# Optimization experiments

Measured on AMD Instinct MI355X. Metric: run time of the kernel, lower is better.

Reference implementation:

```python
import jax, jax.numpy as jnp
import numpy as np

B, E, S = 2, 1024, 2048
H = 16
D_QK = D_V = D_OUT = 1024
NEG = -1e4


def setup_inputs() -> dict:
    key = jax.random.key(0)
    ks = jax.random.split(key, 12)
    q = jax.random.normal(ks[0], (B, E, 1, S), jnp.float32)
    k = jax.random.normal(ks[1], (B, E, 1, S), jnp.float32)
    v = jax.random.normal(ks[2], (B, E, 1, S), jnp.float32)
    # causal qk_mask: (B, src, 1, tgt); src index > tgt index is masked
    causal = jnp.where(jnp.arange(S)[:, None] > jnp.arange(S)[None, :], NEG, 0.0).astype(jnp.float32)
    qk_mask = jnp.broadcast_to(causal[None, :, None, :], (B, S, 1, S))
    k_mask = jnp.zeros((B, S, 1, 1), jnp.float32)
    sc = 1.0 / np.sqrt(E)
    Wq = jax.random.normal(ks[3], (D_QK, E), jnp.float32) * sc
    Wk = jax.random.normal(ks[4], (D_QK, E), jnp.float32) * sc
    Wv = jax.random.normal(ks[5], (D_V, E), jnp.float32) * sc
    Wo = jax.random.normal(ks[6], (D_OUT, D_V), jnp.float32) * sc
    bq = jnp.zeros((D_QK,), jnp.float32)
    bk = jnp.zeros((D_QK,), jnp.float32)
    bv = jnp.zeros((D_V,), jnp.float32)
    bo = jnp.zeros((D_OUT,), jnp.float32)
    return {"q": q, "k": k, "v": v, "qk_mask": qk_mask, "k_mask": k_mask,
            "Wq": Wq, "bq": bq, "Wk": Wk, "bk": bk, "Wv": Wv, "bv": bv,
            "Wo": Wo, "bo": bo}


def reference(q, k, v, qk_mask, k_mask, Wq, bq, Wk, bk, Wv, bv, Wo, bo):
    b, _, _, tq = q.shape
    sk = k.shape[3]
    d_qk, d_v = Wq.shape[0], Wv.shape[0]
    dh, dvh = d_qk // H, d_v // H
    fact = float(dh) ** (-0.5)
    # 1x1 conv projections on (B, C, 1, S) == matmul over channels
    qp = jnp.einsum('oc,bcis->bois', Wq, q) + bq[None, :, None, None]
    kp = jnp.einsum('oc,bcis->bois', Wk, k) + bk[None, :, None, None]
    vp = jnp.einsum('oc,bcis->bois', Wv, v) + bv[None, :, None, None]
    # split heads: channel dim is head-major (contiguous chunks)
    qh = qp[:, :, 0, :].reshape(b, H, dh, tq)
    kh = kp[:, :, 0, :].reshape(b, H, dh, sk)
    vh = vp[:, :, 0, :].reshape(b, H, dvh, sk)
    # scores: (B, H, src, tgt); masks broadcast over heads
    scores = jnp.einsum('bhcq,bhck->bhkq', qh, kh) * fact
    scores = scores + qk_mask[:, None, :, 0, :] + k_mask[:, None, :, 0, 0][..., None]
    w = jax.nn.softmax(scores, axis=2)  # softmax over src (k) axis
    attn = jnp.einsum('bhkq,bhck->bhcq', w, vh).reshape(b, d_v, 1, tq)
    out = jnp.einsum('oc,bcis->bois', Wo, attn) + bo[None, :, None, None]
    return out
```

## Files before the change

kernel.cpp:

```cpp
#include <hip/hip_runtime.h>
#include <hip/hip_bf16.h>
#include <stdint.h>

typedef unsigned short u16;
typedef __attribute__((ext_vector_type(8))) short short8;
typedef __attribute__((ext_vector_type(4))) short short4v;
typedef __attribute__((ext_vector_type(4))) float f32x4;

#define MFMA16(a,b,c) __builtin_amdgcn_mfma_f32_16x16x32_bf16((a),(b),(c),0,0,0)
#define EXP2F(x) __builtin_amdgcn_exp2f(x)

typedef const __attribute__((address_space(1))) void glb_void;
typedef __attribute__((address_space(3))) void lds_void;

__device__ __forceinline__ u16 f2b(float f){
  unsigned u = __float_as_uint(f);
  u += 0x7fffu + ((u>>16)&1u);
  return (u16)(u>>16);
}
__device__ __forceinline__ unsigned pack_bf16(float a, float b){
  __hip_bfloat162 h = __float22bfloat162_rn(make_float2(a,b));
  unsigned u; __builtin_memcpy(&u, &h, 4); return u;
}
__device__ __forceinline__ void gld16(const void* g, void* l){
  __builtin_amdgcn_global_load_lds((glb_void*)g, (lds_void*)l, 16, 0, 0);
}

__device__ __forceinline__ void stage128x64_sw(const u16* g, u16* lds, int gstride, int w, int lane){
  const int sub = lane>>3, c16 = lane&7;
  const int gcol = (c16 ^ sub)<<3;
  #pragma unroll
  for (int i=0;i<4;++i){
    int r0 = (w*4+i)*8;
    gld16(g + (size_t)(r0 + sub)*gstride + gcol, lds + r0*64);
  }
}
__device__ __forceinline__ void stage64x64_sw(const u16* g, u16* lds, int gstride, int w, int lane){
  const int sub = lane>>3, c16 = lane&7;
  const int gcol = (c16 ^ sub)<<3;
  #pragma unroll
  for (int i=0;i<2;++i){
    int r0 = (w*2+i)*8;
    gld16(g + (size_t)(r0 + sub)*gstride + gcol, lds + r0*64);
  }
}
__device__ __forceinline__ const short8* frag64(const u16* lds, int row, int c16){
  return (const short8*)(lds + row*64 + ((c16 ^ (row&7))<<3));
}
__device__ __forceinline__ const short8* frag128(const u16* lds, int row, int c16){
  return (const short8*)(lds + row*128 + ((c16 ^ (row&15))<<3));
}

__global__ __launch_bounds__(256) void prep(
    const float* __restrict__ q, const float* __restrict__ k, const float* __restrict__ v,
    const float* __restrict__ qkm, const float* __restrict__ km,
    const float* __restrict__ Wq, const float* __restrict__ Wk,
    const float* __restrict__ Wv, const float* __restrict__ Wo,
    u16* __restrict__ W16, char* __restrict__ classes,
    u16* __restrict__ qT, u16* __restrict__ kT, u16* __restrict__ vT)
{
  __shared__ __align__(16) float t[64][72];
  const int bx = blockIdx.x, tid = threadIdx.x;
  const int S = 2048, E = 1024, nW = E*E;

  if (bx < 2048){
    const int sel = bx>>9, blk = bx&511;
    const float* src = sel==0?Wq : sel==1?Wk : sel==2?Wv : Wo;
    const float sc = (sel==0) ? 0.18033688f : 1.0f;
    u16* dst = W16 + (size_t)sel*nW;
    int i = (blk*256 + tid)*8;
    float4 a = *(const float4*)(src+i);
    float4 b = *(const float4*)(src+i+4);
    short8 o;
    o[0]=(short)f2b(a.x*sc); o[1]=(short)f2b(a.y*sc); o[2]=(short)f2b(a.z*sc); o[3]=(short)f2b(a.w*sc);
    o[4]=(short)f2b(b.x*sc); o[5]=(short)f2b(b.y*sc); o[6]=(short)f2b(b.z*sc); o[7]=(short)f2b(b.w*sc);
    *(short8*)(dst+i) = o;
  } else if (bx < 4096){
    const int tt = bx - 2048;
    const int b = tt>>10, qi = (tt>>5)&31, ki = tt&31;
    const int k0 = ki*64, q0 = qi*64;
    int az = 1, an = 1;
    #pragma unroll
    for (int p=0;p<4;++p){
      int e = tid + p*256;
      int row = e>>4, c4 = (e&15)*4;
      float kmv = km[(size_t)b*S + k0 + row];
      float4 mv = *(const float4*)&qkm[((size_t)b*S + k0 + row)*S + q0 + c4];
      mv.x += kmv; mv.y += kmv; mv.z += kmv; mv.w += kmv;
      az &= (mv.x==0.f) & (mv.y==0.f) & (mv.z==0.f) & (mv.w==0.f);
      an &= (mv.x<-1e3f) & (mv.y<-1e3f) & (mv.z<-1e3f) & (mv.w<-1e3f);
    }
    const int az_all = __syncthreads_and(az);
    const int an_all = __syncthreads_and(an);
    if (tid==0)
      classes[((size_t)b*32 + qi)*32 + ki] = an_all ? 2 : (az_all ? 0 : 1);
  } else {
    const int tt = bx - 4096;
    const int tensor = tt>>10, r = tt&1023;
    const int b = r>>9, rr = r&511;
    const int c0 = (rr>>5)*64, s0 = (rr&31)*64;
    const float* x = tensor==0 ? q : tensor==1 ? k : v;
    u16* xt = tensor==0 ? qT : tensor==1 ? kT : vT;
    #pragma unroll
    for (int p=0;p<4;++p){
      int e = tid + p*256;
      int row = e>>4, c4 = (e&15)*4;
      *(float4*)&t[row][c4] = *(const float4*)&x[((size_t)b*E + c0 + row)*S + s0 + c4];
    }
    __syncthreads();
    #pragma unroll
    for (int p=0;p<2;++p){
      int e = tid + p*256;
      int row = e>>3, col8 = (e&7)*8;
      short8 o;
      #pragma unroll
      for (int u=0;u<8;++u) o[u] = (short)f2b(t[col8+u][row]);
      *(short8*)&xt[((size_t)b*S + s0 + row)*E + c0 + col8] = o;
    }
  }
}

template<bool F32OUT>
__device__ __forceinline__ void gemm_core(
    const u16* __restrict__ A, const u16* __restrict__ Bt, const float* __restrict__ bias,
    float bscale, void* __restrict__ Cv, size_t cbase, int N, int K, int bias_on_m,
    int m0, int n0, u16* As, u16* Bs)
{
  const int tid = threadIdx.x, w = tid>>6, lane = tid&63;
  const int ln = lane&15, quad = lane>>4;
  const int m0w = (w>>1)*64, n0w = (w&1)*64;
  f32x4 acc[4][4];
  #pragma unroll
  for(int i=0;i<4;++i)
    #pragma unroll
    for(int j=0;j<4;++j) acc[i][j] = f32x4{0.f,0.f,0.f,0.f};

  for (int kc=0; kc<K; kc+=64){
    __syncthreads();
    stage128x64_sw(A  + (size_t)m0*K + kc, As, K, w, lane);
    stage128x64_sw(Bt + (size_t)n0*K + kc, Bs, K, w, lane);
    __syncthreads();
    #pragma unroll
    for (int kk=0; kk<64; kk+=32){
      const int c16 = (kk>>3) + quad;
      short8 af[4], bf[4];
      #pragma unroll
      for (int mt=0;mt<4;++mt) af[mt] = *frag64(As, m0w+mt*16+ln, c16);
      #pragma unroll
      for (int nt=0;nt<4;++nt) bf[nt] = *frag64(Bs, n0w+nt*16+ln, c16);
      #pragma unroll
      for (int mt=0;mt<4;++mt)
        #pragma unroll
        for (int nt=0;nt<4;++nt)
          acc[mt][nt] = MFMA16(af[mt], bf[nt], acc[mt][nt]);
    }
  }
  #pragma unroll
  for (int mt=0;mt<4;++mt){
    #pragma unroll
    for (int nt=0;nt<4;++nt){
      const int col = n0 + n0w + nt*16 + ln;
      const float bn = bias_on_m ? 0.f : bias[col]*bscale;
      #pragma unroll
      for (int r=0;r<4;++r){
        const int row = m0 + m0w + mt*16 + quad*4 + r;
        const float bb = bias_on_m ? bias[row]*bscale : bn;
        const float val = acc[mt][nt][r] + bb;
        const size_t idx = cbase + (size_t)row*N + col;
        if (F32OUT) ((float*)Cv)[idx] = val;
        else        ((u16*)Cv)[idx]   = f2b(val);
      }
    }
  }
}

__global__ __launch_bounds__(256,3) void proj(
    const u16* __restrict__ qT, const u16* __restrict__ kT, const u16* __restrict__ vT,
    const u16* __restrict__ W16,
    const float* __restrict__ bq, const float* __restrict__ bk, const float* __restrict__ bv,
    u16* __restrict__ Qb, u16* __restrict__ Kb, u16* __restrict__ Vb)
{
  __shared__ __align__(16) u16 As[128*64];
  __shared__ __align__(16) u16 Bs[128*64];
  const int bx = blockIdx.x;
  const int zone = bx>>7, r = bx&127;
  const size_t sSE = (size_t)2048*1024;
  const int nW = 1024*1024;
  if (zone < 4){
    const int sel = zone>>1, b = zone&1;
    const int m0 = (r>>3)*128, n0 = (r&7)*128;
    gemm_core<false>((sel? kT : qT) + b*sSE, W16 + (size_t)sel*nW, sel? bk : bq,
                     sel? 1.0f : 0.18033688f, sel? Kb : Qb, b*sSE,
                     1024, 1024, 0, m0, n0, As, Bs);
  } else {
    const int b = zone&1;
    const int m0 = (r>>4)*128, n0 = (r&15)*128;
    gemm_core<false>(W16 + (size_t)2*nW, vT + b*sSE, bv,
                     1.0f, Vb, b*sSE,
                     2048, 1024, 1, m0, n0, As, Bs);
  }
}

__global__ __launch_bounds__(256,4) void gemm_out64(
    const u16* __restrict__ Wo16, const u16* __restrict__ At, const float* __restrict__ bo,
    float* __restrict__ out)
{
  __shared__ __align__(16) u16 As[64*64];
  __shared__ __align__(16) u16 Bs[128*64];
  const int b = blockIdx.z;
  const int m0 = blockIdx.y*64, n0 = blockIdx.x*128;
  const size_t sSE = (size_t)2048*1024;
  const int K = 1024, N = 2048;
  const u16* Bt = At + b*sSE;
  const int tid = threadIdx.x, w = tid>>6, lane = tid&63;
  const int ln = lane&15, quad = lane>>4;
  const int m0w = (w>>1)*32, n0w = (w&1)*64;
  f32x4 acc[2][4];
  #pragma unroll
  for(int i=0;i<2;++i)
    #pragma unroll
    for(int j=0;j<4;++j) acc[i][j] = f32x4{0.f,0.f,0.f,0.f};

  for (int kc=0; kc<K; kc+=64){
    __syncthreads();
    stage64x64_sw (Wo16 + (size_t)m0*K + kc, As, K, w, lane);
    stage128x64_sw(Bt   + (size_t)n0*K + kc, Bs, K, w, lane);
    __syncthreads();
    #pragma unroll
    for (int kk=0; kk<64; kk+=32){
      const int c16 = (kk>>3) + quad;
      short8 af[2], bf[4];
      #pragma unroll
      for (int mt=0;mt<2;++mt) af[mt] = *frag64(As, m0w+mt*16+ln, c16);
      #pragma unroll
      for (int nt=0;nt<4;++nt) bf[nt] = *frag64(Bs, n0w+nt*16+ln, c16);
      #pragma unroll
      for (int mt=0;mt<2;++mt)
        #pragma unroll
        for (int nt=0;nt<4;++nt)
          acc[mt][nt] = MFMA16(af[mt], bf[nt], acc[mt][nt]);
    }
  }
  #pragma unroll
  for (int mt=0;mt<2;++mt){
    #pragma unroll
    for (int nt=0;nt<4;++nt){
      const int col = n0 + n0w + nt*16 + ln;
      #pragma unroll
      for (int r=0;r<4;++r){
        const int row = m0 + m0w + mt*16 + quad*4 + r;
        out[b*sSE + (size_t)row*N + col] = acc[mt][nt][r] + bo[row];
      }
    }
  }
}

__global__ __launch_bounds__(256,2) void attn(
    const u16* __restrict__ Qb, const u16* __restrict__ Kb, const u16* __restrict__ Vb,
    const float* __restrict__ qk_mask, const float* __restrict__ k_mask,
    const char* __restrict__ classes, u16* __restrict__ Ot)
{
  __shared__ __align__(16) u16 Ks[128*64];
  __shared__ __align__(16) u16 Vs[64*128];
  const int bx = blockIdx.x;
  const int st = 31 - (bx>>5);
  const int bh = bx & 31;
  const int b = bh & 1, h = bh >> 1;
  const int tid = threadIdx.x, w = tid>>6, lane = tid&63;
  const int ln = lane&15, quad = lane>>4;
  const int S = 2048;
  const float LOG2E = 1.44269504f, C2 = 16.0f;

  const int qg = st*64 + w*16 + ln;
  short8 qf[2];
  #pragma unroll
  for (int kkI=0;kkI<2;++kkI)
    qf[kkI] = *(const short8*)&Qb[((size_t)b*S + qg)*1024 + h*64 + kkI*32 + quad*8];

  const char* cl = classes + ((size_t)b*32 + st)*32;
  unsigned mMe=0;
  #pragma unroll
  for (int kt=0;kt<16;++kt)
    if (!((cl[2*kt]==2) & (cl[2*kt+1]==2))) mMe |= 1u<<kt;

  float rs = 0.f;
  f32x4 acc[4];
  #pragma unroll
  for (int ct=0;ct<4;++ct) acc[ct] = f32x4{0.f,0.f,0.f,0.f};

  const u16* gK = Kb + ((size_t)b*S)*1024 + h*64;
  const u16* gV = Vb + ((size_t)b*1024 + h*64)*S;
  const int subK = lane>>3, cK = ((lane&7)^subK)<<3;
  const int subV = lane>>4, cV0 = lane&15;

  short8 kreg[4], vreg[4];
  auto issue = [&](int kt){
    const int k0 = kt*128;
    #pragma unroll
    for (int i=0;i<4;++i){
      const int r = (w*4+i)*8 + subK;
      kreg[i] = *(const short8*)(gK + (size_t)(k0 + r)*1024 + cK);
    }
    #pragma unroll
    for (int i=0;i<4;++i){
      const int row = (w*4+i)*4 + subV;
      vreg[i] = *(const short8*)(gV + (size_t)row*S + k0 + ((cV0 ^ (row&15))<<3));
    }
  };
  auto write_lds = [&](){
    #pragma unroll
    for (int i=0;i<4;++i)
      *(short8*)&Ks[(w*4+i)*512 + lane*8] = kreg[i];
    #pragma unroll
    for (int i=0;i<4;++i)
      *(short8*)&Vs[(w*4+i)*512 + lane*8] = vreg[i];
  };

  auto compute = [&](int kt){
    const char c0 = cl[2*kt], c1 = cl[2*kt+1];
    const bool nomask = (c0|c1)==0;
    const int k0 = kt*128;
    unsigned pk[8][2];
    #pragma unroll
    for (int t=0;t<8;++t){
      f32x4 s = f32x4{0.f,0.f,0.f,0.f};
      #pragma unroll
      for (int kkI=0;kkI<2;++kkI)
        s = MFMA16(*frag64(Ks, t*16+ln, kkI*4 + quad), qf[kkI], s);
      float e[4];
      if (nomask){
        #pragma unroll
        for (int r=0;r<4;++r) e[r] = EXP2F(s[r] - C2);
      } else {
        #pragma unroll
        for (int r=0;r<4;++r){
          const int kg = k0 + t*16 + quad*4 + r;
          const float m = qk_mask[((size_t)b*S + kg)*S + qg] + k_mask[(size_t)b*S + kg];
          e[r] = EXP2F(fmaf(m, LOG2E, s[r]) - C2);
        }
      }
      rs += (e[0]+e[1]) + (e[2]+e[3]);
      pk[t][0] = pack_bf16(e[0], e[1]);
      pk[t][1] = pack_bf16(e[2], e[3]);
    }
    const int srcA = (quad&1)*32 + ln, srcB = srcA + 16;
    const bool hi = (quad>>1)&1;
    #pragma unroll
    for (int c=0;c<4;++c){
      unsigned a0 = __shfl((int)pk[2*c][0],   srcA, 64);
      unsigned a1 = __shfl((int)pk[2*c][1],   srcA, 64);
      unsigned a2 = __shfl((int)pk[2*c][0],   srcB, 64);
      unsigned a3 = __shfl((int)pk[2*c][1],   srcB, 64);
      unsigned b0 = __shfl((int)pk[2*c+1][0], srcA, 64);
      unsigned b1 = __shfl((int)pk[2*c+1][1], srcA, 64);
      unsigned b2 = __shfl((int)pk[2*c+1][0], srcB, 64);
      unsigned b3 = __shfl((int)pk[2*c+1][1], srcB, 64);
      short8 pf;
      ((unsigned*)&pf)[0] = hi ? b0 : a0;
      ((unsigned*)&pf)[1] = hi ? b1 : a1;
      ((unsigned*)&pf)[2] = hi ? b2 : a2;
      ((unsigned*)&pf)[3] = hi ? b3 : a3;
      __builtin_amdgcn_s_setprio(1);
      #pragma unroll
      for (int ct=0;ct<4;++ct)
        acc[ct] = MFMA16(*frag128(Vs, ct*16+ln, c*4 + quad), pf, acc[ct]);
      __builtin_amdgcn_s_setprio(0);
    }
  };

  int cur = mMe ? (__ffs(mMe)-1) : 16;
  if (cur < 16) issue(cur);
  while (cur < 16){
    const unsigned above = mMe & (0xfffffffeu << cur);
    const int nxt = above ? (__ffs(above)-1) : 16;
    __builtin_amdgcn_s_barrier();
    __builtin_amdgcn_sched_barrier(0);
    write_lds();
    if (nxt < 16) issue(nxt);
    asm volatile("s_waitcnt lgkmcnt(0)" ::: "memory");
    __builtin_amdgcn_s_barrier();
    __builtin_amdgcn_sched_barrier(0);
    compute(cur);
    cur = nxt;
  }

  rs += __shfl_xor(rs, 16, 64);
  rs += __shfl_xor(rs, 32, 64);
  const float rinv = 1.0f / rs;
  #pragma unroll
  for (int ct=0;ct<4;++ct){
    short4v o4;
    #pragma unroll
    for (int r=0;r<4;++r) o4[r] = (short)f2b(acc[ct][r] * rinv);
    *(short4v*)&Ot[((size_t)b*S + qg)*1024 + h*64 + ct*16 + quad*4] = o4;
  }
}

extern "C" void kernel_launch(void* const* d_in, const int* in_sizes, int n_in,
                              void* d_out, int out_size, void* d_ws, size_t ws_size,
                              hipStream_t stream)
{
  const float* q   = (const float*)d_in[0];
  const float* k   = (const float*)d_in[1];
  const float* v   = (const float*)d_in[2];
  const float* qkm = (const float*)d_in[3];
  const float* km  = (const float*)d_in[4];
  const float* Wq  = (const float*)d_in[5];
  const float* bq  = (const float*)d_in[6];
  const float* Wk  = (const float*)d_in[7];
  const float* bk  = (const float*)d_in[8];
  const float* Wv  = (const float*)d_in[9];
  const float* bv  = (const float*)d_in[10];
  const float* Wo  = (const float*)d_in[11];
  const float* bo  = (const float*)d_in[12];
  float* out = (float*)d_out;

  const size_t nAct = (size_t)2*2048*1024;
  const int   nW   = 1024*1024;

  u16* A0 = (u16*)d_ws;
  u16* A1 = A0 + nAct;
  u16* A2 = A1 + nAct;
  u16* A3 = A2 + nAct;
  u16* A4 = A3 + nAct;
  u16* A5 = A4 + nAct;
  u16* W16 = A5 + nAct;
  char* classes = (char*)(W16 + (size_t)4*nW);
  u16* Wo16 = W16 + (size_t)3*nW;

  dim3 blk(256);
  prep      <<<dim3(7168), blk, 0, stream>>>(q, k, v, qkm, km, Wq, Wk, Wv, Wo,
                                             W16, classes, A0, A1, A2);
  proj      <<<dim3(768),  blk, 0, stream>>>(A0, A1, A2, W16, bq, bk, bv, A3, A4, A5);
  attn      <<<dim3(1024), blk, 0, stream>>>(A3, A4, A5, qkm, km, classes, A0);
  gemm_out64<<<dim3(16,16,2), blk, 0, stream>>>(Wo16, A0, bo, out);
}
```

Baseline: 237.6 us.

## Split long causal query tiles across two blocks and merge partials in combine kernel

The upper half of query tiles (the longest causal rows) is now split into two key-range chunks, each handled by its own block, so the attention grid grows to 1536 blocks with better load balance. Split blocks write unnormalized fp32 partial accumulators and row sums to workspace, and a new combine kernel adds them, normalizes and writes bf16 output. This relies on softmax using a fixed offset rather than a running max, so partials can be summed directly. The cost is an extra launch plus fp32 partial traffic through reused workspace.

```diff
diff --git a/kernel.cpp b/kernel.cpp
--- a/kernel.cpp
+++ b/kernel.cpp
@@ -258,13 +258,21 @@
 __global__ __launch_bounds__(256,2) void attn(
     const u16* __restrict__ Qb, const u16* __restrict__ Kb, const u16* __restrict__ Vb,
     const float* __restrict__ qk_mask, const float* __restrict__ k_mask,
-    const char* __restrict__ classes, u16* __restrict__ Ot)
+    const char* __restrict__ classes, u16* __restrict__ Ot,
+    float* __restrict__ part, float* __restrict__ rsp)
 {
   __shared__ __align__(16) u16 Ks[128*64];
   __shared__ __align__(16) u16 Vs[64*128];
   const int bx = blockIdx.x;
-  const int st = 31 - (bx>>5);
-  const int bh = bx & 31;
+  const bool split = bx < 1024;
+  int st, bh, chunk;
+  if (split){
+    const int p = bx>>1; chunk = bx&1;
+    st = 31 - (p>>5); bh = p&31;
+  } else {
+    const int d = bx - 1024; chunk = 0;
+    st = 15 - (d>>5); bh = d&31;
+  }
   const int b = bh & 1, h = bh >> 1;
   const int tid = threadIdx.x, w = tid>>6, lane = tid&63;
   const int ln = lane&15, quad = lane>>4;
@@ -282,6 +290,15 @@
   #pragma unroll
   for (int kt=0;kt<16;++kt)
     if (!((cl[2*kt]==2) & (cl[2*kt+1]==2))) mMe |= 1u<<kt;
+
+  unsigned mUse = mMe;
+  if (split){
+    const int n = __popc(mMe);
+    const int n0 = (n+1)>>1;
+    unsigned hi = mMe;
+    for (int i=0;i<n0;++i) hi &= hi-1;
+    mUse = chunk ? hi : (mMe & ~hi);
+  }
 
   float rs = 0.f;
   f32x4 acc[4];
@@ -368,10 +385,10 @@
     }
   };
 
-  int cur = mMe ? (__ffs(mMe)-1) : 16;
+  int cur = mUse ? (__ffs(mUse)-1) : 16;
   if (cur < 16) issue(cur);
   while (cur < 16){
-    const unsigned above = mMe & (0xfffffffeu << cur);
+    const unsigned above = mUse & (0xfffffffeu << cur);
     const int nxt = above ? (__ffs(above)-1) : 16;
     __builtin_amdgcn_s_barrier();
     __builtin_amdgcn_sched_barrier(0);
@@ -386,14 +403,42 @@
 
   rs += __shfl_xor(rs, 16, 64);
   rs += __shfl_xor(rs, 32, 64);
-  const float rinv = 1.0f / rs;
-  #pragma unroll
-  for (int ct=0;ct<4;++ct){
-    short4v o4;
-    #pragma unroll
-    for (int r=0;r<4;++r) o4[r] = (short)f2b(acc[ct][r] * rinv);
-    *(short4v*)&Ot[((size_t)b*S + qg)*1024 + h*64 + ct*16 + quad*4] = o4;
-  }
+  if (split){
+    float* pacc = part + (size_t)bx*4096;
+    const int row = w*16 + ln;
+    #pragma unroll
+    for (int ct=0;ct<4;++ct)
+      *(f32x4*)&pacc[row*64 + ct*16 + quad*4] = acc[ct];
+    if (quad==0) rsp[(size_t)bx*64 + row] = rs;
+  } else {
+    const float rinv = 1.0f / rs;
+    #pragma unroll
+    for (int ct=0;ct<4;++ct){
+      short4v o4;
+      #pragma unroll
+      for (int r=0;r<4;++r) o4[r] = (short)f2b(acc[ct][r] * rinv);
+      *(short4v*)&Ot[((size_t)b*S + qg)*1024 + h*64 + ct*16 + quad*4] = o4;
+    }
+  }
+}
+
+__global__ __launch_bounds__(256) void comb(
+    const float* __restrict__ part, const float* __restrict__ rsp, u16* __restrict__ Ot)
+{
+  const int p = blockIdx.x;
+  const int st = 31 - (p>>5), bh = p&31, b = bh&1, h = bh>>1;
+  const int tid = threadIdx.x;
+  const int row = tid>>2, cg = (tid&3)*16;
+  const float* a0 = part + (size_t)(2*p)*4096 + row*64 + cg;
+  const float* a1 = a0 + 4096;
+  const float rsum = rsp[(size_t)(2*p)*64 + row] + rsp[(size_t)(2*p+1)*64 + row];
+  const float rinv = 1.0f / rsum;
+  u16 o[16];
+  #pragma unroll
+  for (int i=0;i<16;++i) o[i] = f2b((a0[i] + a1[i]) * rinv);
+  u16* dst = Ot + ((size_t)b*2048 + st*64 + row)*1024 + h*64 + cg;
+  *(short8*)dst     = *(short8*)&o[0];
+  *(short8*)(dst+8) = *(short8*)&o[8];
 }
 
 extern "C" void kernel_launch(void* const* d_in, const int* in_sizes, int n_in,
@@ -426,12 +471,16 @@
   u16* A5 = A4 + nAct;
   u16* W16 = A5 + nAct;
   char* classes = (char*)(W16 + (size_t)4*nW);
+  float* partp  = (float*)A1;
+  float* rspp   = (float*)(classes + 4096);
   u16* Wo16 = W16 + (size_t)3*nW;
 
   dim3 blk(256);
   prep      <<<dim3(7168), blk, 0, stream>>>(q, k, v, qkm, km, Wq, Wk, Wv, Wo,
                                              W16, classes, A0, A1, A2);
   proj      <<<dim3(768),  blk, 0, stream>>>(A0, A1, A2, W16, bq, bk, bv, A3, A4, A5);
-  attn      <<<dim3(1024), blk, 0, stream>>>(A3, A4, A5, qkm, km, classes, A0);
+  attn      <<<dim3(1536), blk, 0, stream>>>(A3, A4, A5, qkm, km, classes, A0,
+                                             partp, rspp);
+  comb      <<<dim3(512),  blk, 0, stream>>>(partp, rspp, A0);
   gemm_out64<<<dim3(16,16,2), blk, 0, stream>>>(Wo16, A0, bo, out);
 }
```

New measurement: 257.4 us. 8.3% more time.

## Prefetch GEMM tiles through registers to overlap global loads with MFMA

Applied to the files above, without the earlier changes.

Replaces the direct global-to-LDS staging in the projection and output GEMMs with a register-staged software pipeline. The next K-chunk's global loads are issued into registers while the current chunk is computed, then written to LDS after a barrier. This is meant to hide global memory latency behind the MFMA work. The extra prefetch registers raise register pressure, so the launch-bounds occupancy hints are lowered.

```diff
diff --git a/kernel.cpp b/kernel.cpp
--- a/kernel.cpp
+++ b/kernel.cpp
@@ -26,24 +26,6 @@
   __builtin_amdgcn_global_load_lds((glb_void*)g, (lds_void*)l, 16, 0, 0);
 }
 
-__device__ __forceinline__ void stage128x64_sw(const u16* g, u16* lds, int gstride, int w, int lane){
-  const int sub = lane>>3, c16 = lane&7;
-  const int gcol = (c16 ^ sub)<<3;
-  #pragma unroll
-  for (int i=0;i<4;++i){
-    int r0 = (w*4+i)*8;
-    gld16(g + (size_t)(r0 + sub)*gstride + gcol, lds + r0*64);
-  }
-}
-__device__ __forceinline__ void stage64x64_sw(const u16* g, u16* lds, int gstride, int w, int lane){
-  const int sub = lane>>3, c16 = lane&7;
-  const int gcol = (c16 ^ sub)<<3;
-  #pragma unroll
-  for (int i=0;i<2;++i){
-    int r0 = (w*2+i)*8;
-    gld16(g + (size_t)(r0 + sub)*gstride + gcol, lds + r0*64);
-  }
-}
 __device__ __forceinline__ const short8* frag64(const u16* lds, int row, int c16){
   return (const short8*)(lds + row*64 + ((c16 ^ (row&7))<<3));
 }
@@ -129,17 +111,39 @@
   const int tid = threadIdx.x, w = tid>>6, lane = tid&63;
   const int ln = lane&15, quad = lane>>4;
   const int m0w = (w>>1)*64, n0w = (w&1)*64;
+  const int sub = lane>>3, gcol = ((lane&7)^sub)<<3;
   f32x4 acc[4][4];
   #pragma unroll
   for(int i=0;i<4;++i)
     #pragma unroll
     for(int j=0;j<4;++j) acc[i][j] = f32x4{0.f,0.f,0.f,0.f};
 
+  short8 areg[4], breg[4];
+  auto issue = [&](int kc){
+    #pragma unroll
+    for (int i=0;i<4;++i){
+      const int r0 = (w*4+i)*8 + sub;
+      areg[i] = *(const short8*)(A  + (size_t)(m0 + r0)*K + kc + gcol);
+      breg[i] = *(const short8*)(Bt + (size_t)(n0 + r0)*K + kc + gcol);
+    }
+  };
+  auto write_lds = [&](){
+    #pragma unroll
+    for (int i=0;i<4;++i){
+      *(short8*)&As[(w*4+i)*512 + lane*8] = areg[i];
+      *(short8*)&Bs[(w*4+i)*512 + lane*8] = breg[i];
+    }
+  };
+
+  issue(0);
   for (int kc=0; kc<K; kc+=64){
-    __syncthreads();
-    stage128x64_sw(A  + (size_t)m0*K + kc, As, K, w, lane);
-    stage128x64_sw(Bt + (size_t)n0*K + kc, Bs, K, w, lane);
-    __syncthreads();
+    __builtin_amdgcn_s_barrier();
+    __builtin_amdgcn_sched_barrier(0);
+    write_lds();
+    if (kc+64 < K) issue(kc+64);
+    asm volatile("s_waitcnt lgkmcnt(0)" ::: "memory");
+    __builtin_amdgcn_s_barrier();
+    __builtin_amdgcn_sched_barrier(0);
     #pragma unroll
     for (int kk=0; kk<64; kk+=32){
       const int c16 = (kk>>3) + quad;
@@ -174,7 +178,7 @@
   }
 }
 
-__global__ __launch_bounds__(256,3) void proj(
+__global__ __launch_bounds__(256,2) void proj(
     const u16* __restrict__ qT, const u16* __restrict__ kT, const u16* __restrict__ vT,
     const u16* __restrict__ W16,
     const float* __restrict__ bq, const float* __restrict__ bk, const float* __restrict__ bv,
@@ -201,7 +205,7 @@
   }
 }
 
-__global__ __launch_bounds__(256,4) void gemm_out64(
+__global__ __launch_bounds__(256,3) void gemm_out64(
     const u16* __restrict__ Wo16, const u16* __restrict__ At, const float* __restrict__ bo,
     float* __restrict__ out)
 {
@@ -215,17 +219,44 @@
   const int tid = threadIdx.x, w = tid>>6, lane = tid&63;
   const int ln = lane&15, quad = lane>>4;
   const int m0w = (w>>1)*32, n0w = (w&1)*64;
+  const int sub = lane>>3, gcol = ((lane&7)^sub)<<3;
   f32x4 acc[2][4];
   #pragma unroll
   for(int i=0;i<2;++i)
     #pragma unroll
     for(int j=0;j<4;++j) acc[i][j] = f32x4{0.f,0.f,0.f,0.f};
 
+  short8 areg[2], breg[4];
+  auto issue = [&](int kc){
+    #pragma unroll
+    for (int i=0;i<2;++i){
+      const int r0 = (w*2+i)*8 + sub;
+      areg[i] = *(const short8*)(Wo16 + (size_t)(m0 + r0)*K + kc + gcol);
+    }
+    #pragma unroll
+    for (int i=0;i<4;++i){
+      const int r0 = (w*4+i)*8 + sub;
+      breg[i] = *(const short8*)(Bt + (size_t)(n0 + r0)*K + kc + gcol);
+    }
+  };
+  auto write_lds = [&](){
+    #pragma unroll
+    for (int i=0;i<2;++i)
+      *(short8*)&As[(w*2+i)*512 + lane*8] = areg[i];
+    #pragma unroll
+    for (int i=0;i<4;++i)
+      *(short8*)&Bs[(w*4+i)*512 + lane*8] = breg[i];
+  };
+
+  issue(0);
   for (int kc=0; kc<K; kc+=64){
-    __syncthreads();
-    stage64x64_sw (Wo16 + (size_t)m0*K + kc, As, K, w, lane);
-    stage128x64_sw(Bt   + (size_t)n0*K + kc, Bs, K, w, lane);
-    __syncthreads();
+    __builtin_amdgcn_s_barrier();
+    __builtin_amdgcn_sched_barrier(0);
+    write_lds();
+    if (kc+64 < K) issue(kc+64);
+    asm volatile("s_waitcnt lgkmcnt(0)" ::: "memory");
+    __builtin_amdgcn_s_barrier();
+    __builtin_amdgcn_sched_barrier(0);
     #pragma unroll
     for (int kk=0; kk<64; kk+=32){
       const int c16 = (kk>>3) + quad;
```

Result: no change. 237.5 us (-0.0%).

## Classify causal mask tiles analytically and stage P through LDS instead of shuffles

Applied to the files above, without the earlier changes.

The prep kernel adds a tile class (3) for tiles whose mask matches an exact causal pattern. The attention kernel then computes the mask from indices for those tiles instead of loading qk_mask from global memory. The P-fragment transpose now goes through a swizzled per-wave LDS buffer rather than 8 cross-lane shuffles per chunk, and the block-to-head mapping is permuted. This cuts global mask traffic on diagonal tiles and shuffle cost, at the price of extra LDS and a three-way class check in prep.

```diff
diff --git a/kernel.cpp b/kernel.cpp
--- a/kernel.cpp
+++ b/kernel.cpp
@@ -62,6 +62,7 @@
   __shared__ __align__(16) float t[64][72];
   const int bx = blockIdx.x, tid = threadIdx.x;
   const int S = 2048, E = 1024, nW = E*E;
+  const float NEG = -1e4f;
 
   if (bx < 2048){
     const int sel = bx>>9, blk = bx&511;
@@ -79,21 +80,29 @@
     const int tt = bx - 2048;
     const int b = tt>>10, qi = (tt>>5)&31, ki = tt&31;
     const int k0 = ki*64, q0 = qi*64;
-    int az = 1, an = 1;
+    int az = 1, an = 1, ac = 1;
     #pragma unroll
     for (int p=0;p<4;++p){
       int e = tid + p*256;
       int row = e>>4, c4 = (e&15)*4;
-      float kmv = km[(size_t)b*S + k0 + row];
-      float4 mv = *(const float4*)&qkm[((size_t)b*S + k0 + row)*S + q0 + c4];
+      const int kg = k0 + row;
+      float kmv = km[(size_t)b*S + kg];
+      float4 mv = *(const float4*)&qkm[((size_t)b*S + kg)*S + q0 + c4];
       mv.x += kmv; mv.y += kmv; mv.z += kmv; mv.w += kmv;
       az &= (mv.x==0.f) & (mv.y==0.f) & (mv.z==0.f) & (mv.w==0.f);
       an &= (mv.x<-1e3f) & (mv.y<-1e3f) & (mv.z<-1e3f) & (mv.w<-1e3f);
+      const float e0 = (kg > q0+c4+0) ? NEG : 0.f;
+      const float e1 = (kg > q0+c4+1) ? NEG : 0.f;
+      const float e2 = (kg > q0+c4+2) ? NEG : 0.f;
+      const float e3 = (kg > q0+c4+3) ? NEG : 0.f;
+      ac &= (mv.x==e0) & (mv.y==e1) & (mv.z==e2) & (mv.w==e3);
     }
     const int az_all = __syncthreads_and(az);
     const int an_all = __syncthreads_and(an);
+    const int ac_all = __syncthreads_and(ac);
     if (tid==0)
-      classes[((size_t)b*32 + qi)*32 + ki] = an_all ? 2 : (az_all ? 0 : 1);
+      classes[((size_t)b*32 + qi)*32 + ki] =
+          an_all ? 2 : (az_all ? 0 : (ac_all ? 3 : 1));
   } else {
     const int tt = bx - 4096;
     const int tensor = tt>>10, r = tt&1023;
@@ -262,9 +271,10 @@
 {
   __shared__ __align__(16) u16 Ks[128*64];
   __shared__ __align__(16) u16 Vs[64*128];
+  __shared__ __align__(16) u16 Ps[4*16*128];
   const int bx = blockIdx.x;
   const int st = 31 - (bx>>5);
-  const int bh = bx & 31;
+  const int bh = (bx&7)*4 + ((bx>>3)&3);
   const int b = bh & 1, h = bh >> 1;
   const int tid = threadIdx.x, w = tid>>6, lane = tid&63;
   const int ln = lane&15, quad = lane>>4;
@@ -288,6 +298,9 @@
   #pragma unroll
   for (int ct=0;ct<4;++ct) acc[ct] = f32x4{0.f,0.f,0.f,0.f};
 
+  char* Pbase = (char*)(Ps + w*16*128) + ln*256;
+  const int rsw = (ln&7)<<4;
+
   const u16* gK = Kb + ((size_t)b*S)*1024 + h*64;
   const u16* gV = Vb + ((size_t)b*1024 + h*64)*S;
   const int subK = lane>>3, cK = ((lane&7)^subK)<<3;
@@ -319,8 +332,8 @@
   auto compute = [&](int kt){
     const char c0 = cl[2*kt], c1 = cl[2*kt+1];
     const bool nomask = (c0|c1)==0;
+    const bool analytic = (c0!=1) & (c1!=1);
     const int k0 = kt*128;
-    unsigned pk[8][2];
     #pragma unroll
     for (int t=0;t<8;++t){
       f32x4 s = f32x4{0.f,0.f,0.f,0.f};
@@ -331,6 +344,12 @@
       if (nomask){
         #pragma unroll
         for (int r=0;r<4;++r) e[r] = EXP2F(s[r] - C2);
+      } else if (analytic){
+        #pragma unroll
+        for (int r=0;r<4;++r){
+          const int kg = k0 + t*16 + quad*4 + r;
+          e[r] = (kg <= qg) ? EXP2F(s[r] - C2) : 0.f;
+        }
       } else {
         #pragma unroll
         for (int r=0;r<4;++r){
@@ -340,26 +359,14 @@
         }
       }
       rs += (e[0]+e[1]) + (e[2]+e[3]);
-      pk[t][0] = pack_bf16(e[0], e[1]);
-      pk[t][1] = pack_bf16(e[2], e[3]);
-    }
-    const int srcA = (quad&1)*32 + ln, srcB = srcA + 16;
-    const bool hi = (quad>>1)&1;
+      uint2 pp;
+      pp.x = pack_bf16(e[0], e[1]);
+      pp.y = pack_bf16(e[2], e[3]);
+      *(uint2*)(Pbase + ((t*32 + quad*8) ^ rsw)) = pp;
+    }
     #pragma unroll
     for (int c=0;c<4;++c){
-      unsigned a0 = __shfl((int)pk[2*c][0],   srcA, 64);
-      unsigned a1 = __shfl((int)pk[2*c][1],   srcA, 64);
-      unsigned a2 = __shfl((int)pk[2*c][0],   srcB, 64);
-      unsigned a3 = __shfl((int)pk[2*c][1],   srcB, 64);
-      unsigned b0 = __shfl((int)pk[2*c+1][0], srcA, 64);
-      unsigned b1 = __shfl((int)pk[2*c+1][1], srcA, 64);
-      unsigned b2 = __shfl((int)pk[2*c+1][0], srcB, 64);
-      unsigned b3 = __shfl((int)pk[2*c+1][1], srcB, 64);
-      short8 pf;
-      ((unsigned*)&pf)[0] = hi ? b0 : a0;
-      ((unsigned*)&pf)[1] = hi ? b1 : a1;
-      ((unsigned*)&pf)[2] = hi ? b2 : a2;
-      ((unsigned*)&pf)[3] = hi ? b3 : a3;
+      const short8 pf = *(const short8*)(Pbase + ((c*64 + quad*16) ^ rsw));
       __builtin_amdgcn_s_setprio(1);
       #pragma unroll
       for (int ct=0;ct<4;++ct)
```

After: 229.1 us, median of 2. 3.6% less time.
